# Kernel tuning notes

Measured on AMD Instinct MI355X. Metric: run time of the kernel, lower is better.

## Reference

```python
import math
import jax, jax.numpy as jnp
import numpy as np

EPS = 1e-5
D_MODEL, N_HEADS, D_HEAD = 512, 8, 64


def make_signed_quant(num_bits):
    Qn = -2 ** (num_bits - 1)
    Qp = 2 ** (num_bits - 1) - 1

    @jax.custom_vjp
    def quant(x, alpha):
        a = jnp.maximum(alpha, EPS)
        return jnp.clip(jnp.round(x / a), Qn, Qp) * a

    def fwd(x, alpha):
        a = jnp.maximum(alpha, EPS)
        return jnp.clip(jnp.round(x / a), Qn, Qp) * a, (x, a)

    def bwd(res, g):
        x, a = res
        qw = x / a
        small = (qw < Qn).astype(g.dtype)
        big = (qw > Qp).astype(g.dtype)
        mid = 1.0 - small - big
        gs = 1.0 / math.sqrt(x.size * Qp)
        ga = jnp.sum((small * Qn + big * Qp + mid * (jnp.round(qw) - qw)) * g) * gs
        return mid * g, ga.reshape(())

    quant.defvjp(fwd, bwd)
    return quant


def make_unsigned_quant(num_bits):
    Qp = 2 ** num_bits - 1

    @jax.custom_vjp
    def quant(x, alpha):
        a = jnp.maximum(alpha, EPS)
        mn = jnp.min(x)
        return jnp.clip(jnp.round((x - mn) / a), 0, Qp) * a + mn

    def fwd(x, alpha):
        a = jnp.maximum(alpha, EPS)
        mn = jnp.min(x)
        return jnp.clip(jnp.round((x - mn) / a), 0, Qp) * a + mn, (x - mn, a)

    def bwd(res, g):
        xs, a = res
        qw = xs / a
        small = (qw < 0).astype(g.dtype)
        big = (qw > Qp).astype(g.dtype)
        mid = 1.0 - small - big
        gs = 1.0 / math.sqrt(xs.size * Qp)
        ga = jnp.sum((big * Qp + mid * (jnp.round(qw) - qw)) * g) * gs
        return mid * g, ga.reshape(())

    quant.defvjp(fwd, bwd)
    return quant


def _bwn_body(w):
    # layerwise BWN: sign(w - mean(w)) * mean(|w|)
    m = jnp.mean(jnp.abs(w))
    e = jnp.mean(w)
    return jnp.sign(w - e) * m


@jax.custom_vjp
def bwn(w):
    return _bwn_body(w)


def _bwn_fwd(w):
    return _bwn_body(w), None


def _bwn_bwd(_, g):
    return (g,)  # straight-through


bwn.defvjp(_bwn_fwd, _bwn_bwd)

sig4 = make_signed_quant(4)
sig8 = make_signed_quant(8)  # the output QuantizeLinear uses default input_bits=8
uns4 = make_unsigned_quant(4)


def layernorm(x, g, b):
    mu = jnp.mean(x, axis=-1, keepdims=True)
    var = jnp.var(x, axis=-1, keepdims=True)
    return (x - mu) / jnp.sqrt(var + 1e-5) * g + b


def attention_forward(q, k, v, Wq, Wk, Wv, Wo, bq, bk, bv, ln_g, ln_b,
                      aq_in, ak_in, av_in, a_cq, a_ck, a_cv, a_cattn, ao_in):
    B, S, _ = q.shape
    # QuantizeLinear: 4-bit elastic act quant + BWN binary weights, NO bias; then LearnableBias add
    Q = sig4(q, aq_in) @ bwn(Wq).T + bq
    K = sig4(k, ak_in) @ bwn(Wk).T + bk
    V = sig4(v, av_in) @ bwn(Wv).T + bv

    def split(x):  # [B,S,H*d] -> [B,H,S,d]
        return jnp.transpose(x.reshape(B, -1, N_HEADS, D_HEAD), (0, 2, 1, 3))

    Q, K, V = split(Q), split(K), split(V)
    Q = sig4(Q, a_cq)
    K = sig4(K, a_ck)
    V = sig4(V, a_cv)
    scores = jnp.einsum('bhqd,bhkd->bhqk', Q, K) / math.sqrt(D_HEAD)
    # NOTE: original calls scores.masked_fill(mask==0, -1e9) WITHOUT assignment,
    # so the mask has no effect on the math; replicated faithfully.
    attn = jax.nn.softmax(scores, axis=-1)
    attn = uns4(attn, a_cattn)
    ctx = jnp.einsum('bhqk,bhkd->bhqd', attn, V)
    # faithful to original `.view(B, S, H*d)` on the [B,H,S,d] tensor (no head transpose)
    ctx = ctx.reshape(B, S, N_HEADS * D_HEAD)
    out = sig8(ctx, ao_in) @ bwn(Wo).T
    return layernorm(q + out, ln_g, ln_b), scores


def setup_inputs() -> dict:
    key = jax.random.key(0)
    ks = jax.random.split(key, 8)
    B, S, D = 4, 1024, 512
    f = jnp.float32
    return {
        'q': jax.random.normal(ks[0], (B, S, D), f),
        'k': jax.random.normal(ks[1], (B, S, D), f),
        'v': jax.random.normal(ks[2], (B, S, D), f),
        'mask': jnp.ones((B, 1, S, S), jnp.int32),
        'Wq': jax.random.normal(ks[3], (D, D), f) * 0.02,
        'Wk': jax.random.normal(ks[4], (D, D), f) * 0.02,
        'Wv': jax.random.normal(ks[5], (D, D), f) * 0.02,
        'Wo': jax.random.normal(ks[6], (D, D), f) * 0.02,
        'bq': jnp.zeros((D,), f),
        'bk': jnp.zeros((D,), f),
        'bv': jnp.zeros((D,), f),
        'ln_g': jnp.ones((D,), f),
        'ln_b': jnp.zeros((D,), f),
        'aq_in': jnp.asarray(0.5, f),
        'ak_in': jnp.asarray(0.5, f),
        'av_in': jnp.asarray(0.5, f),
        'a_cq': jnp.asarray(0.2, f),
        'a_ck': jnp.asarray(0.2, f),
        'a_cv': jnp.asarray(0.2, f),
        'a_cattn': jnp.asarray(0.002, f),
        'ao_in': jnp.asarray(0.01, f),
    }


def reference(q, k, v, mask, Wq, Wk, Wv, Wo, bq, bk, bv, ln_g, ln_b,
              aq_in, ak_in, av_in, a_cq, a_ck, a_cv, a_cattn, ao_in):
    # mask is structurally unused (original masked_fill is not in-place and discarded)
    return attention_forward(q, k, v, Wq, Wk, Wv, Wo, bq, bk, bv, ln_g, ln_b,
                             aq_in, ak_in, av_in, a_cq, a_ck, a_cv, a_cattn, ao_in)
```

## Files before the change

### kernel.cpp

```cpp
#include <hip/hip_runtime.h>
#include <math.h>
#include <stdint.h>

#define EPSQ 1e-5f
#define WELEM 262144
#define OUT0N 2097152

#define O_WSUM   0
#define O_WABS   16
#define O_MN     32
#define O_COLSUM 64
#define O_WSIGNS 16384
#define O_KQ     (O_WSIGNS + 8*WELEM)
#define O_CTXQ   O_KQ
#define O_KK     (O_KQ + 4194304)
#define O_VT     (O_KK + 4194304)
#define O_RMAX   (O_VT + 4194304)
#define O_RSUM   (O_RMAX + 131072)
#define O_OUTB   (O_RSUM + 131072)
#define O_RCAND  O_OUTB

#define AS 72

typedef __bf16 bf16x8 __attribute__((ext_vector_type(8)));
typedef __bf16 bf16x4 __attribute__((ext_vector_type(4)));
typedef float  floatx4 __attribute__((ext_vector_type(4)));

__device__ __forceinline__ float clampf(float x, float lo, float hi) {
  return fminf(fmaxf(x, lo), hi);
}

__global__ void k_init(float* wsum, float* wabs, float* colsum) {
  int t = threadIdx.x;
  if (t < 4) { wsum[t] = 0.f; wabs[t] = 0.f; }
  for (int i = t; i < 2048; i += 256) colsum[i] = 0.f;
}

__global__ void k_wstats(const float* Wq, const float* Wk, const float* Wv, const float* Wo,
                         float* wsum, float* wabs) {
  __shared__ float s1[256], s2[256];
  int w = blockIdx.x >> 6;
  const float* W = (w == 0) ? Wq : (w == 1) ? Wk : (w == 2) ? Wv : Wo;
  int base = (blockIdx.x & 63) * 4096;
  float s = 0.f, sa = 0.f;
  for (int i = threadIdx.x; i < 4096; i += 256) {
    float x = W[base + i];
    s += x; sa += fabsf(x);
  }
  s1[threadIdx.x] = s; s2[threadIdx.x] = sa; __syncthreads();
  for (int o = 128; o > 0; o >>= 1) {
    if (threadIdx.x < o) { s1[threadIdx.x] += s1[threadIdx.x + o]; s2[threadIdx.x] += s2[threadIdx.x + o]; }
    __syncthreads();
  }
  if (threadIdx.x == 0) { atomicAdd(&wsum[w], s1[0]); atomicAdd(&wabs[w], s2[0]); }
}

__global__ void k_sign(const float* Wq, const float* Wk, const float* Wv, const float* Wo,
                       const float* wsum, __bf16* wsigns) {
  int idx = blockIdx.x * 256 + threadIdx.x;
  int w = idx >> 18;
  int pos = idx & (WELEM - 1);
  const float* W = (w == 0) ? Wq : (w == 1) ? Wk : (w == 2) ? Wv : Wo;
  float e = wsum[w] * (1.0f / 262144.0f);
  float x = W[pos];
  wsigns[idx] = (__bf16)(float)((x > e) - (x < e));
}

__global__ __launch_bounds__(256) void k_proj(
    const float* q, const float* kin, const float* vin,
    const float* bq, const float* bk, const float* bv,
    const float* aq, const float* ak, const float* av,
    const float* acq, const float* ack, const float* acv,
    const __bf16* wsigns, const float* wabs,
    __bf16* kqo, __bf16* kko, __bf16* vto, float* colsum) {
  __shared__ __align__(16) __bf16 As[64][AS];
  __shared__ __align__(16) __bf16 Bs[64][AS];
  int z = blockIdx.z;
  const float* X    = (z == 0) ? q   : (z == 1) ? kin : vin;
  const float* bias = (z == 0) ? bq  : (z == 1) ? bk  : bv;
  const float* aip  = (z == 0) ? aq  : (z == 1) ? ak  : av;
  const float* ahp  = (z == 0) ? acq : (z == 1) ? ack : acv;
  float a_in = fmaxf(aip[0], EPSQ);
  float a_hd = fmaxf(ahp[0], EPSQ);
  float m_w  = wabs[z] * (1.0f / 262144.0f);
  const __bf16* S = wsigns + (size_t)z * WELEM;

  int n0 = blockIdx.x * 64;
  int f0 = blockIdx.y * 64;
  int t = threadIdx.x;
  int lane = t & 63, w = t >> 6, quad = lane >> 4, l16 = lane & 15;
  int c4 = (t & 15) * 4, mb = t >> 4;
  int e16 = (t & 3) * 16, mrow = t >> 2;
  floatx4 acc[4];
#pragma unroll
  for (int nt = 0; nt < 4; ++nt) acc[nt] = (floatx4){0.f, 0.f, 0.f, 0.f};

  for (int k0 = 0; k0 < 512; k0 += 64) {
#pragma unroll
    for (int j = 0; j < 4; ++j) {
      int m = mb + j * 16;
      float4 x = *(const float4*)&X[(size_t)(n0 + m) * 512 + k0 + c4];
      bf16x4 av = { (__bf16)clampf(rintf(x.x / a_in), -8.f, 7.f),
                    (__bf16)clampf(rintf(x.y / a_in), -8.f, 7.f),
                    (__bf16)clampf(rintf(x.z / a_in), -8.f, 7.f),
                    (__bf16)clampf(rintf(x.w / a_in), -8.f, 7.f) };
      *(bf16x4*)&As[m][c4] = av;
    }
    {
      const __bf16* src = &S[(size_t)(f0 + mrow) * 512 + k0 + e16];
      *(bf16x8*)&Bs[mrow][e16]     = *(const bf16x8*)src;
      *(bf16x8*)&Bs[mrow][e16 + 8] = *(const bf16x8*)(src + 8);
    }
    __syncthreads();
#pragma unroll
    for (int kh = 0; kh < 64; kh += 32) {
      bf16x8 a = *(const bf16x8*)&As[w * 16 + l16][kh + quad * 8];
#pragma unroll
      for (int nt = 0; nt < 4; ++nt) {
        bf16x8 b = *(const bf16x8*)&Bs[nt * 16 + l16][kh + quad * 8];
        acc[nt] = __builtin_amdgcn_mfma_f32_16x16x32_bf16(a, b, acc[nt], 0, 0, 0);
      }
    }
    __syncthreads();
  }
  float s_am = a_in * m_w;
  if (z != 2) {
    __bf16* outp = (z == 0) ? kqo : kko;
#pragma unroll
    for (int nt = 0; nt < 4; ++nt) {
      int f = f0 + nt * 16 + l16;
      int h = f >> 6, dd = f & 63;
      float bia = bias[f];
#pragma unroll
      for (int r = 0; r < 4; ++r) {
        int n = n0 + w * 16 + quad * 4 + r;
        int b = n >> 10, srow = n & 1023;
        float P = s_am * acc[nt][r] + bia;
        float hq = clampf(rintf(P / a_hd), -8.f, 7.f);
        outp[(size_t)((b * 8 + h) * 1024 + srow) * 64 + dd] = (__bf16)hq;
      }
    }
  } else {
    int b = n0 >> 10;
    int srow0 = (n0 & 1023) + w * 16 + quad * 4;
#pragma unroll
    for (int nt = 0; nt < 4; ++nt) {
      int f = f0 + nt * 16 + l16;
      int h = f >> 6, dd = f & 63;
      int bh = b * 8 + h;
      float bia = bias[f];
      float part = 0.f;
      bf16x4 pack;
#pragma unroll
      for (int r = 0; r < 4; ++r) {
        float P = s_am * acc[nt][r] + bia;
        float hq = clampf(rintf(P / a_hd), -8.f, 7.f);
        pack[r] = (__bf16)hq;
        part += hq;
      }
      *(bf16x4*)&vto[((size_t)bh * 64 + dd) * 1024 + srow0] = pack;
      atomicAdd(&colsum[bh * 64 + dd], part);
    }
  }
}

__global__ __launch_bounds__(256) void k_qks(
    const __bf16* kq, const __bf16* kkv,
    const float* acq, const float* ack,
    float* scores, float* rmax, float* rsum, float* rcand) {
  __shared__ __align__(16) __bf16 As[64][AS];
  __shared__ __align__(16) __bf16 Bs[64][AS];
  int bh = blockIdx.y;
  int q0 = blockIdx.x * 64;
  const __bf16* A  = kq  + (size_t)bh * 65536;
  const __bf16* Bp = kkv + (size_t)bh * 65536;
  float* Sp = scores + ((size_t)bh * 1024 + q0) * 1024;
  int t = threadIdx.x;
  int lane = t & 63, w = t >> 6, quad = lane >> 4, l16 = lane & 15;
  int e16 = (t & 3) * 16, mrow = t >> 2;
  float sc = fmaxf(acq[0], EPSQ) * fmaxf(ack[0], EPSQ) * 0.125f;

  {
    const __bf16* src = &A[(q0 + mrow) * 64 + e16];
    *(bf16x8*)&As[mrow][e16]     = *(const bf16x8*)src;
    *(bf16x8*)&As[mrow][e16 + 8] = *(const bf16x8*)(src + 8);
  }
  float m_run[4], l_run[4], mn_run[4];
#pragma unroll
  for (int rr = 0; rr < 4; ++rr) { m_run[rr] = -INFINITY; l_run[rr] = 0.f; mn_run[rr] = INFINITY; }

  for (int ct = 0; ct < 16; ++ct) {
    __syncthreads();
    {
      const __bf16* src = &Bp[(ct * 64 + mrow) * 64 + e16];
      *(bf16x8*)&Bs[mrow][e16]     = *(const bf16x8*)src;
      *(bf16x8*)&Bs[mrow][e16 + 8] = *(const bf16x8*)(src + 8);
    }
    __syncthreads();
    floatx4 acc[4];
#pragma unroll
    for (int nt = 0; nt < 4; ++nt) acc[nt] = (floatx4){0.f, 0.f, 0.f, 0.f};
#pragma unroll
    for (int kh = 0; kh < 64; kh += 32) {
      bf16x8 a = *(const bf16x8*)&As[w * 16 + l16][kh + quad * 8];
#pragma unroll
      for (int nt = 0; nt < 4; ++nt) {
        bf16x8 b = *(const bf16x8*)&Bs[nt * 16 + l16][kh + quad * 8];
        acc[nt] = __builtin_amdgcn_mfma_f32_16x16x32_bf16(a, b, acc[nt], 0, 0, 0);
      }
    }
#pragma unroll
    for (int rr = 0; rr < 4; ++rr) {
      int row = w * 16 + quad * 4 + rr;
      float v[4];
#pragma unroll
      for (int nt = 0; nt < 4; ++nt) {
        v[nt] = sc * acc[nt][rr];
        Sp[(size_t)row * 1024 + ct * 64 + nt * 16 + l16] = v[nt];
      }
      float tmax = fmaxf(fmaxf(v[0], v[1]), fmaxf(v[2], v[3]));
      float tmin = fminf(fminf(v[0], v[1]), fminf(v[2], v[3]));
      mn_run[rr] = fminf(mn_run[rr], tmin);
      float mnew = fmaxf(m_run[rr], tmax);
      float s = 0.f;
#pragma unroll
      for (int nt = 0; nt < 4; ++nt) s += expf(v[nt] - mnew);
      l_run[rr] = l_run[rr] * expf(m_run[rr] - mnew) + s;
      m_run[rr] = mnew;
    }
  }
#pragma unroll
  for (int o = 1; o < 16; o <<= 1) {
#pragma unroll
    for (int rr = 0; rr < 4; ++rr) {
      float mo = __shfl_xor(m_run[rr], o);
      float lo = __shfl_xor(l_run[rr], o);
      float mnew = fmaxf(m_run[rr], mo);
      l_run[rr] = l_run[rr] * expf(m_run[rr] - mnew) + lo * expf(mo - mnew);
      m_run[rr] = mnew;
      mn_run[rr] = fminf(mn_run[rr], __shfl_xor(mn_run[rr], o));
    }
  }
  if (l16 == 0) {
#pragma unroll
    for (int rr = 0; rr < 4; ++rr) {
      int r = bh * 1024 + q0 + w * 16 + quad * 4 + rr;
      rmax[r] = m_run[rr];
      rsum[r] = l_run[rr];
      rcand[r] = expf(mn_run[rr] - m_run[rr]) * (1.0f / l_run[rr]);
    }
  }
}

__global__ __launch_bounds__(1024) void k_minred(const float* rcand, float* mnf) {
  __shared__ float red[1024];
  float mn = INFINITY;
  for (int i = threadIdx.x; i < 32768; i += 1024) mn = fminf(mn, rcand[i]);
  red[threadIdx.x] = mn; __syncthreads();
  for (int o = 512; o > 0; o >>= 1) {
    if (threadIdx.x < o) red[threadIdx.x] = fminf(red[threadIdx.x], red[threadIdx.x + o]);
    __syncthreads();
  }
  if (threadIdx.x == 0) mnf[0] = red[0];
}

__global__ __launch_bounds__(256) void k_pv(
    const float* scores, const float* rmax, const float* rsum,
    const float* mnf, const float* colsum, const __bf16* vt,
    const float* acattn, const float* acv, const float* ao,
    __bf16* ctxq) {
  __shared__ __align__(16) __bf16 As[32][AS];
  __shared__ __align__(16) __bf16 Bs[64][AS];
  int bh = blockIdx.y;
  int m0 = blockIdx.x * 32;
  float mn = mnf[0];
  float a_att = fmaxf(acattn[0], EPSQ);
  float a_v   = fmaxf(acv[0], EPSQ);
  float a_o   = fmaxf(ao[0], EPSQ);
  const float* Sp  = scores + (size_t)bh * 1048576;
  const __bf16* Vt = vt + (size_t)bh * 65536;
  int t = threadIdx.x;
  int lane = t & 63, w = t >> 6, quad = lane >> 4, l16 = lane & 15;
  int mt = w & 1, np = w >> 1;
  int c4 = (t & 15) * 4, mb = t >> 4;
  int e16 = (t & 3) * 16, mrow = t >> 2;
  float rm[2], rs[2];
#pragma unroll
  for (int j = 0; j < 2; ++j) {
    int r = bh * 1024 + m0 + mb + j * 16;
    rm[j] = rmax[r]; rs[j] = rsum[r];
  }
  floatx4 acc[2];
  acc[0] = (floatx4){0.f, 0.f, 0.f, 0.f};
  acc[1] = (floatx4){0.f, 0.f, 0.f, 0.f};

  for (int k0 = 0; k0 < 1024; k0 += 64) {
#pragma unroll
    for (int j = 0; j < 2; ++j) {
      int m = mb + j * 16;
      float4 s4 = *(const float4*)&Sp[(size_t)(m0 + m) * 1024 + k0 + c4];
      float inv = 1.0f / rs[j];
      bf16x4 av = {
        (__bf16)clampf(rintf((expf(s4.x - rm[j]) * inv - mn) / a_att), 0.f, 15.f),
        (__bf16)clampf(rintf((expf(s4.y - rm[j]) * inv - mn) / a_att), 0.f, 15.f),
        (__bf16)clampf(rintf((expf(s4.z - rm[j]) * inv - mn) / a_att), 0.f, 15.f),
        (__bf16)clampf(rintf((expf(s4.w - rm[j]) * inv - mn) / a_att), 0.f, 15.f) };
      *(bf16x4*)&As[m][c4] = av;
    }
    {
      const __bf16* src = &Vt[(size_t)mrow * 1024 + k0 + e16];
      *(bf16x8*)&Bs[mrow][e16]     = *(const bf16x8*)src;
      *(bf16x8*)&Bs[mrow][e16 + 8] = *(const bf16x8*)(src + 8);
    }
    __syncthreads();
#pragma unroll
    for (int kh = 0; kh < 64; kh += 32) {
      bf16x8 a = *(const bf16x8*)&As[mt * 16 + l16][kh + quad * 8];
#pragma unroll
      for (int j = 0; j < 2; ++j) {
        bf16x8 b = *(const bf16x8*)&Bs[(np * 2 + j) * 16 + l16][kh + quad * 8];
        acc[j] = __builtin_amdgcn_mfma_f32_16x16x32_bf16(a, b, acc[j], 0, 0, 0);
      }
    }
    __syncthreads();
  }
  float sc  = a_att * a_v;
  float mnv = mn * a_v;
  int b = bh >> 3, h = bh & 7;
#pragma unroll
  for (int j = 0; j < 2; ++j) {
    int dd = (np * 2 + j) * 16 + l16;
    float cs = colsum[bh * 64 + dd];
#pragma unroll
    for (int r = 0; r < 4; ++r) {
      int srow = m0 + mt * 16 + quad * 4 + r;
      float ctx = sc * acc[j][r] + mnv * cs;
      float c8 = clampf(rintf(ctx / a_o), -128.f, 127.f);
      ctxq[(size_t)b * 524288 + (size_t)(h * 128 + (srow >> 3)) * 512 + (srow & 7) * 64 + dd] = (__bf16)c8;
    }
  }
}

__global__ __launch_bounds__(256) void k_outg(
    const __bf16* ctxq, const __bf16* signs_o,
    const float* wabs, const float* ao, float* outb) {
  __shared__ __align__(16) __bf16 As[64][AS];
  __shared__ __align__(16) __bf16 Bs[64][AS];
  int n0 = blockIdx.x * 64, f0 = blockIdx.y * 64;
  int t = threadIdx.x;
  int lane = t & 63, w = t >> 6, quad = lane >> 4, l16 = lane & 15;
  int e16 = (t & 3) * 16, mrow = t >> 2;
  floatx4 acc[4];
#pragma unroll
  for (int nt = 0; nt < 4; ++nt) acc[nt] = (floatx4){0.f, 0.f, 0.f, 0.f};
  for (int k0 = 0; k0 < 512; k0 += 64) {
    {
      const __bf16* sa = &ctxq[(size_t)(n0 + mrow) * 512 + k0 + e16];
      const __bf16* sb = &signs_o[(size_t)(f0 + mrow) * 512 + k0 + e16];
      *(bf16x8*)&As[mrow][e16]     = *(const bf16x8*)sa;
      *(bf16x8*)&As[mrow][e16 + 8] = *(const bf16x8*)(sa + 8);
      *(bf16x8*)&Bs[mrow][e16]     = *(const bf16x8*)sb;
      *(bf16x8*)&Bs[mrow][e16 + 8] = *(const bf16x8*)(sb + 8);
    }
    __syncthreads();
#pragma unroll
    for (int kh = 0; kh < 64; kh += 32) {
      bf16x8 a = *(const bf16x8*)&As[w * 16 + l16][kh + quad * 8];
#pragma unroll
      for (int nt = 0; nt < 4; ++nt) {
        bf16x8 b = *(const bf16x8*)&Bs[nt * 16 + l16][kh + quad * 8];
        acc[nt] = __builtin_amdgcn_mfma_f32_16x16x32_bf16(a, b, acc[nt], 0, 0, 0);
      }
    }
    __syncthreads();
  }
  float scale = fmaxf(ao[0], EPSQ) * (wabs[3] * (1.0f / 262144.0f));
#pragma unroll
  for (int nt = 0; nt < 4; ++nt)
#pragma unroll
    for (int r = 0; r < 4; ++r)
      outb[(size_t)(n0 + w * 16 + quad * 4 + r) * 512 + f0 + nt * 16 + l16] = scale * acc[nt][r];
}

__global__ __launch_bounds__(256) void k_ln(
    const float* q, const float* outb, const float* g, const float* bb, float* out0) {
  __shared__ float red[256];
  int r = blockIdx.x, t = threadIdx.x;
  const float* qp = q + (size_t)r * 512;
  const float* op = outb + (size_t)r * 512;
  float y0 = qp[t] + op[t];
  float y1 = qp[t + 256] + op[t + 256];
  red[t] = y0 + y1; __syncthreads();
  for (int o = 128; o > 0; o >>= 1) { if (t < o) red[t] += red[t + o]; __syncthreads(); }
  float mu = red[0] * (1.0f / 512.0f); __syncthreads();
  float d0 = y0 - mu, d1 = y1 - mu;
  red[t] = d0 * d0 + d1 * d1; __syncthreads();
  for (int o = 128; o > 0; o >>= 1) { if (t < o) red[t] += red[t + o]; __syncthreads(); }
  float var = red[0] * (1.0f / 512.0f);
  float den = sqrtf(var + 1e-5f);
  out0[(size_t)r * 512 + t]       = d0 / den * g[t] + bb[t];
  out0[(size_t)r * 512 + t + 256] = d1 / den * g[t + 256] + bb[t + 256];
}

extern "C" void kernel_launch(void* const* d_in, const int* in_sizes, int n_in,
                              void* d_out, int out_size, void* d_ws, size_t ws_size,
                              hipStream_t stream) {
  const float* q   = (const float*)d_in[0];
  const float* k   = (const float*)d_in[1];
  const float* v   = (const float*)d_in[2];
  const float* Wq  = (const float*)d_in[4];
  const float* Wk  = (const float*)d_in[5];
  const float* Wv  = (const float*)d_in[6];
  const float* Wo  = (const float*)d_in[7];
  const float* bq  = (const float*)d_in[8];
  const float* bk  = (const float*)d_in[9];
  const float* bv  = (const float*)d_in[10];
  const float* lng = (const float*)d_in[11];
  const float* lnb = (const float*)d_in[12];
  const float* aq  = (const float*)d_in[13];
  const float* ak  = (const float*)d_in[14];
  const float* av  = (const float*)d_in[15];
  const float* acq = (const float*)d_in[16];
  const float* ack = (const float*)d_in[17];
  const float* acv = (const float*)d_in[18];
  const float* aca = (const float*)d_in[19];
  const float* ao  = (const float*)d_in[20];

  char* ws = (char*)d_ws;
  float*  wsum   = (float*)(ws + O_WSUM);
  float*  wabs   = (float*)(ws + O_WABS);
  float*  mnf    = (float*)(ws + O_MN);
  float*  colsum = (float*)(ws + O_COLSUM);
  __bf16* wsigns = (__bf16*)(ws + O_WSIGNS);
  __bf16* kqb    = (__bf16*)(ws + O_KQ);
  __bf16* kkb    = (__bf16*)(ws + O_KK);
  __bf16* vtb    = (__bf16*)(ws + O_VT);
  float*  rmax   = (float*)(ws + O_RMAX);
  float*  rsum   = (float*)(ws + O_RSUM);
  float*  rcand  = (float*)(ws + O_RCAND);
  __bf16* ctxq   = (__bf16*)(ws + O_CTXQ);
  float*  outb   = (float*)(ws + O_OUTB);

  float* out0   = (float*)d_out;
  float* scores = (float*)d_out + OUT0N;

  k_init<<<1, 256, 0, stream>>>(wsum, wabs, colsum);
  k_wstats<<<256, 256, 0, stream>>>(Wq, Wk, Wv, Wo, wsum, wabs);
  k_sign<<<4096, 256, 0, stream>>>(Wq, Wk, Wv, Wo, wsum, wsigns);
  k_proj<<<dim3(64, 8, 3), 256, 0, stream>>>(q, k, v, bq, bk, bv, aq, ak, av,
                                             acq, ack, acv, wsigns, wabs,
                                             kqb, kkb, vtb, colsum);
  k_qks<<<dim3(16, 32), 256, 0, stream>>>(kqb, kkb, acq, ack, scores, rmax, rsum, rcand);
  k_minred<<<1, 1024, 0, stream>>>(rcand, mnf);
  k_pv<<<dim3(32, 32), 256, 0, stream>>>(scores, rmax, rsum, mnf, colsum, vtb,
                                         aca, acv, ao, ctxq);
  k_outg<<<dim3(64, 8), 256, 0, stream>>>(ctxq, wsigns + 3 * WELEM, wabs, ao, outb);
  k_ln<<<4096, 256, 0, stream>>>(q, outb, lng, lnb, out0);
}
```

Measured before the change: 378.5 us.

## Prefetch next tiles into registers and pre-quantize inputs in a separate kernel

Adds a k_qx kernel that quantizes q/k/v once into bf16 buffers, so k_proj no longer re-quantizes the fp32 input for every one of its 8 output-column blocks. It also applies register double-buffering to the GEMM loops in k_proj, k_qks, k_pv and k_outg: the next tile is loaded from global memory while the current one is computed, and the trailing barrier is replaced by a leading one. The cost is an extra kernel launch plus 12 MB of workspace traffic, and higher register pressure in the GEMM kernels.

```diff
diff --git a/kernel.cpp b/kernel.cpp
--- a/kernel.cpp
+++ b/kernel.cpp
@@ -11,8 +11,11 @@
 #define O_MN     32
 #define O_COLSUM 64
 #define O_WSIGNS 16384
-#define O_KQ     (O_WSIGNS + 8*WELEM)
-#define O_CTXQ   O_KQ
+#define O_QLV    (O_WSIGNS + 8*WELEM)
+#define O_CTXQ   O_QLV
+#define O_KLV    (O_QLV + 4194304)
+#define O_VLV    (O_KLV + 4194304)
+#define O_KQ     (O_VLV + 4194304)
 #define O_KK     (O_KQ + 4194304)
 #define O_VT     (O_KK + 4194304)
 #define O_RMAX   (O_VT + 4194304)
@@ -25,6 +28,14 @@
 typedef __bf16 bf16x8 __attribute__((ext_vector_type(8)));
 typedef __bf16 bf16x4 __attribute__((ext_vector_type(4)));
 typedef float  floatx4 __attribute__((ext_vector_type(4)));
+
+struct pre2 { bf16x8 lo, hi; };
+__device__ __forceinline__ pre2 ldb16(const __bf16* p) {
+  pre2 r; r.lo = *(const bf16x8*)p; r.hi = *(const bf16x8*)(p + 8); return r;
+}
+__device__ __forceinline__ void stb16(__bf16* p, pre2 r) {
+  *(bf16x8*)p = r.lo; *(bf16x8*)(p + 8) = r.hi;
+}
 
 __device__ __forceinline__ float clampf(float x, float lo, float hi) {
   return fminf(fmaxf(x, lo), hi);
@@ -66,8 +77,31 @@
   wsigns[idx] = (__bf16)(float)((x > e) - (x < e));
 }
 
+__global__ __launch_bounds__(256) void k_qx(
+    const float* q, const float* kin, const float* vin,
+    const float* aq, const float* ak, const float* av,
+    __bf16* qlv, __bf16* klv, __bf16* vlv) {
+  int z = blockIdx.y;
+  const float* X = (z == 0) ? q : (z == 1) ? kin : vin;
+  const float* ap = (z == 0) ? aq : (z == 1) ? ak : av;
+  __bf16* O = (z == 0) ? qlv : (z == 1) ? klv : vlv;
+  float a = fmaxf(ap[0], EPSQ);
+  size_t i = ((size_t)blockIdx.x * 256 + threadIdx.x) * 8;
+  float4 x0 = *(const float4*)&X[i];
+  float4 x1 = *(const float4*)&X[i + 4];
+  bf16x8 o = { (__bf16)clampf(rintf(x0.x / a), -8.f, 7.f),
+               (__bf16)clampf(rintf(x0.y / a), -8.f, 7.f),
+               (__bf16)clampf(rintf(x0.z / a), -8.f, 7.f),
+               (__bf16)clampf(rintf(x0.w / a), -8.f, 7.f),
+               (__bf16)clampf(rintf(x1.x / a), -8.f, 7.f),
+               (__bf16)clampf(rintf(x1.y / a), -8.f, 7.f),
+               (__bf16)clampf(rintf(x1.z / a), -8.f, 7.f),
+               (__bf16)clampf(rintf(x1.w / a), -8.f, 7.f) };
+  *(bf16x8*)&O[i] = o;
+}
+
 __global__ __launch_bounds__(256) void k_proj(
-    const float* q, const float* kin, const float* vin,
+    const __bf16* qlv, const __bf16* klv, const __bf16* vlv,
     const float* bq, const float* bk, const float* bv,
     const float* aq, const float* ak, const float* av,
     const float* acq, const float* ack, const float* acv,
@@ -76,7 +110,7 @@
   __shared__ __align__(16) __bf16 As[64][AS];
   __shared__ __align__(16) __bf16 Bs[64][AS];
   int z = blockIdx.z;
-  const float* X    = (z == 0) ? q   : (z == 1) ? kin : vin;
+  const __bf16* X   = (z == 0) ? qlv : (z == 1) ? klv : vlv;
   const float* bias = (z == 0) ? bq  : (z == 1) ? bk  : bv;
   const float* aip  = (z == 0) ? aq  : (z == 1) ? ak  : av;
   const float* ahp  = (z == 0) ? acq : (z == 1) ? ack : acv;
@@ -89,28 +123,19 @@
   int f0 = blockIdx.y * 64;
   int t = threadIdx.x;
   int lane = t & 63, w = t >> 6, quad = lane >> 4, l16 = lane & 15;
-  int c4 = (t & 15) * 4, mb = t >> 4;
   int e16 = (t & 3) * 16, mrow = t >> 2;
+  const __bf16* ap = &X[(size_t)(n0 + mrow) * 512 + e16];
+  const __bf16* bp = &S[(size_t)(f0 + mrow) * 512 + e16];
   floatx4 acc[4];
 #pragma unroll
   for (int nt = 0; nt < 4; ++nt) acc[nt] = (floatx4){0.f, 0.f, 0.f, 0.f};
 
+  pre2 pa = ldb16(ap), pb = ldb16(bp);
   for (int k0 = 0; k0 < 512; k0 += 64) {
-#pragma unroll
-    for (int j = 0; j < 4; ++j) {
-      int m = mb + j * 16;
-      float4 x = *(const float4*)&X[(size_t)(n0 + m) * 512 + k0 + c4];
-      bf16x4 av = { (__bf16)clampf(rintf(x.x / a_in), -8.f, 7.f),
-                    (__bf16)clampf(rintf(x.y / a_in), -8.f, 7.f),
-                    (__bf16)clampf(rintf(x.z / a_in), -8.f, 7.f),
-                    (__bf16)clampf(rintf(x.w / a_in), -8.f, 7.f) };
-      *(bf16x4*)&As[m][c4] = av;
-    }
-    {
-      const __bf16* src = &S[(size_t)(f0 + mrow) * 512 + k0 + e16];
-      *(bf16x8*)&Bs[mrow][e16]     = *(const bf16x8*)src;
-      *(bf16x8*)&Bs[mrow][e16 + 8] = *(const bf16x8*)(src + 8);
-    }
+    if (k0) __syncthreads();
+    stb16(&As[mrow][e16], pa);
+    stb16(&Bs[mrow][e16], pb);
+    if (k0 + 64 < 512) { pa = ldb16(ap + k0 + 64); pb = ldb16(bp + k0 + 64); }
     __syncthreads();
 #pragma unroll
     for (int kh = 0; kh < 64; kh += 32) {
@@ -121,7 +146,6 @@
         acc[nt] = __builtin_amdgcn_mfma_f32_16x16x32_bf16(a, b, acc[nt], 0, 0, 0);
       }
     }
-    __syncthreads();
   }
   float s_am = a_in * m_w;
   if (z != 2) {
@@ -180,22 +204,16 @@
   int e16 = (t & 3) * 16, mrow = t >> 2;
   float sc = fmaxf(acq[0], EPSQ) * fmaxf(ack[0], EPSQ) * 0.125f;
 
-  {
-    const __bf16* src = &A[(q0 + mrow) * 64 + e16];
-    *(bf16x8*)&As[mrow][e16]     = *(const bf16x8*)src;
-    *(bf16x8*)&As[mrow][e16 + 8] = *(const bf16x8*)(src + 8);
-  }
+  stb16(&As[mrow][e16], ldb16(&A[(q0 + mrow) * 64 + e16]));
   float m_run[4], l_run[4], mn_run[4];
 #pragma unroll
   for (int rr = 0; rr < 4; ++rr) { m_run[rr] = -INFINITY; l_run[rr] = 0.f; mn_run[rr] = INFINITY; }
 
+  pre2 pb = ldb16(&Bp[mrow * 64 + e16]);
   for (int ct = 0; ct < 16; ++ct) {
-    __syncthreads();
-    {
-      const __bf16* src = &Bp[(ct * 64 + mrow) * 64 + e16];
-      *(bf16x8*)&Bs[mrow][e16]     = *(const bf16x8*)src;
-      *(bf16x8*)&Bs[mrow][e16 + 8] = *(const bf16x8*)(src + 8);
-    }
+    if (ct) __syncthreads();
+    stb16(&Bs[mrow][e16], pb);
+    if (ct < 15) pb = ldb16(&Bp[((ct + 1) * 64 + mrow) * 64 + e16]);
     __syncthreads();
     floatx4 acc[4];
 #pragma unroll
@@ -294,23 +312,30 @@
   acc[0] = (floatx4){0.f, 0.f, 0.f, 0.f};
   acc[1] = (floatx4){0.f, 0.f, 0.f, 0.f};
 
+  float4 ps[2];
+#pragma unroll
+  for (int j = 0; j < 2; ++j)
+    ps[j] = *(const float4*)&Sp[(size_t)(m0 + mb + j * 16) * 1024 + c4];
+  pre2 pvb = ldb16(&Vt[(size_t)mrow * 1024 + e16]);
+
   for (int k0 = 0; k0 < 1024; k0 += 64) {
+    if (k0) __syncthreads();
 #pragma unroll
     for (int j = 0; j < 2; ++j) {
-      int m = mb + j * 16;
-      float4 s4 = *(const float4*)&Sp[(size_t)(m0 + m) * 1024 + k0 + c4];
       float inv = 1.0f / rs[j];
       bf16x4 av = {
-        (__bf16)clampf(rintf((expf(s4.x - rm[j]) * inv - mn) / a_att), 0.f, 15.f),
-        (__bf16)clampf(rintf((expf(s4.y - rm[j]) * inv - mn) / a_att), 0.f, 15.f),
-        (__bf16)clampf(rintf((expf(s4.z - rm[j]) * inv - mn) / a_att), 0.f, 15.f),
-        (__bf16)clampf(rintf((expf(s4.w - rm[j]) * inv - mn) / a_att), 0.f, 15.f) };
-      *(bf16x4*)&As[m][c4] = av;
-    }
-    {
-      const __bf16* src = &Vt[(size_t)mrow * 1024 + k0 + e16];
-      *(bf16x8*)&Bs[mrow][e16]     = *(const bf16x8*)src;
-      *(bf16x8*)&Bs[mrow][e16 + 8] = *(const bf16x8*)(src + 8);
+        (__bf16)clampf(rintf((expf(ps[j].x - rm[j]) * inv - mn) / a_att), 0.f, 15.f),
+        (__bf16)clampf(rintf((expf(ps[j].y - rm[j]) * inv - mn) / a_att), 0.f, 15.f),
+        (__bf16)clampf(rintf((expf(ps[j].z - rm[j]) * inv - mn) / a_att), 0.f, 15.f),
+        (__bf16)clampf(rintf((expf(ps[j].w - rm[j]) * inv - mn) / a_att), 0.f, 15.f) };
+      *(bf16x4*)&As[mb + j * 16][c4] = av;
+    }
+    stb16(&Bs[mrow][e16], pvb);
+    if (k0 + 64 < 1024) {
+#pragma unroll
+      for (int j = 0; j < 2; ++j)
+        ps[j] = *(const float4*)&Sp[(size_t)(m0 + mb + j * 16) * 1024 + k0 + 64 + c4];
+      pvb = ldb16(&Vt[(size_t)mrow * 1024 + k0 + 64 + e16]);
     }
     __syncthreads();
 #pragma unroll
@@ -322,7 +347,6 @@
         acc[j] = __builtin_amdgcn_mfma_f32_16x16x32_bf16(a, b, acc[j], 0, 0, 0);
       }
     }
-    __syncthreads();
   }
   float sc  = a_att * a_v;
   float mnv = mn * a_v;
@@ -350,18 +374,17 @@
   int t = threadIdx.x;
   int lane = t & 63, w = t >> 6, quad = lane >> 4, l16 = lane & 15;
   int e16 = (t & 3) * 16, mrow = t >> 2;
+  const __bf16* ap = &ctxq[(size_t)(n0 + mrow) * 512 + e16];
+  const __bf16* bp = &signs_o[(size_t)(f0 + mrow) * 512 + e16];
   floatx4 acc[4];
 #pragma unroll
   for (int nt = 0; nt < 4; ++nt) acc[nt] = (floatx4){0.f, 0.f, 0.f, 0.f};
+  pre2 pa = ldb16(ap), pb = ldb16(bp);
   for (int k0 = 0; k0 < 512; k0 += 64) {
-    {
-      const __bf16* sa = &ctxq[(size_t)(n0 + mrow) * 512 + k0 + e16];
-      const __bf16* sb = &signs_o[(size_t)(f0 + mrow) * 512 + k0 + e16];
-      *(bf16x8*)&As[mrow][e16]     = *(const bf16x8*)sa;
-      *(bf16x8*)&As[mrow][e16 + 8] = *(const bf16x8*)(sa + 8);
-      *(bf16x8*)&Bs[mrow][e16]     = *(const bf16x8*)sb;
-      *(bf16x8*)&Bs[mrow][e16 + 8] = *(const bf16x8*)(sb + 8);
-    }
+    if (k0) __syncthreads();
+    stb16(&As[mrow][e16], pa);
+    stb16(&Bs[mrow][e16], pb);
+    if (k0 + 64 < 512) { pa = ldb16(ap + k0 + 64); pb = ldb16(bp + k0 + 64); }
     __syncthreads();
 #pragma unroll
     for (int kh = 0; kh < 64; kh += 32) {
@@ -372,7 +395,6 @@
         acc[nt] = __builtin_amdgcn_mfma_f32_16x16x32_bf16(a, b, acc[nt], 0, 0, 0);
       }
     }
-    __syncthreads();
   }
   float scale = fmaxf(ao[0], EPSQ) * (wabs[3] * (1.0f / 262144.0f));
 #pragma unroll
@@ -432,6 +454,9 @@
   float*  mnf    = (float*)(ws + O_MN);
   float*  colsum = (float*)(ws + O_COLSUM);
   __bf16* wsigns = (__bf16*)(ws + O_WSIGNS);
+  __bf16* qlv    = (__bf16*)(ws + O_QLV);
+  __bf16* klv    = (__bf16*)(ws + O_KLV);
+  __bf16* vlv    = (__bf16*)(ws + O_VLV);
   __bf16* kqb    = (__bf16*)(ws + O_KQ);
   __bf16* kkb    = (__bf16*)(ws + O_KK);
   __bf16* vtb    = (__bf16*)(ws + O_VT);
@@ -447,7 +472,8 @@
   k_init<<<1, 256, 0, stream>>>(wsum, wabs, colsum);
   k_wstats<<<256, 256, 0, stream>>>(Wq, Wk, Wv, Wo, wsum, wabs);
   k_sign<<<4096, 256, 0, stream>>>(Wq, Wk, Wv, Wo, wsum, wsigns);
-  k_proj<<<dim3(64, 8, 3), 256, 0, stream>>>(q, k, v, bq, bk, bv, aq, ak, av,
+  k_qx<<<dim3(1024, 3), 256, 0, stream>>>(q, k, v, aq, ak, av, qlv, klv, vlv);
+  k_proj<<<dim3(64, 8, 3), 256, 0, stream>>>(qlv, klv, vlv, bq, bk, bv, aq, ak, av,
                                              acq, ack, acv, wsigns, wabs,
                                              kqb, kkb, vtb, colsum);
   k_qks<<<dim3(16, 32), 256, 0, stream>>>(kqb, kkb, acq, ack, scores, rmax, rsum, rcand);
```

Measured after the change: 346.8 us. -8.4%, faster.
